# Kernel optimization log

Hardware: AMD Instinct MI355X
Metric: run time of the kernel (lower is better)

## Reference

```python
import jax, jax.numpy as jnp
import numpy as np

N_BLOCKS = 128
B0, B1 = 32, 32
COND_DIM = 0
IN_FEAT = B1 * N_BLOCKS + COND_DIM   # 4096
OUT_FEAT = B0 * N_BLOCKS             # 4096
BATCH = 2048


def _make_masks():
    # block-diagonal mask and strictly-lower block-triangular mask (int32)
    diag = np.kron(np.eye(N_BLOCKS, dtype=np.int32), np.ones((B0, B1), np.int32))
    tril = np.kron(np.tril(np.ones((N_BLOCKS, N_BLOCKS), np.int32), -1),
                   np.ones((B0, B1), np.int32))
    return jnp.asarray(diag), jnp.asarray(tril)


def setup_inputs() -> dict:
    key = jax.random.key(0)
    kx, kw, kb, ks = jax.random.split(key, 4)
    b_diag_mask, b_tril_mask = _make_masks()
    # glorot-like init, masked to the allowed sparsity pattern (as in __init__)
    scale = float(np.sqrt(2.0 / (IN_FEAT + OUT_FEAT)))
    W = jax.random.normal(kw, (OUT_FEAT, IN_FEAT), jnp.float32) * scale
    W = W * (b_diag_mask + b_tril_mask).astype(jnp.float32)
    bias = (jax.random.uniform(kb, (OUT_FEAT,), jnp.float32) - 0.5) * (2.0 / np.sqrt(OUT_FEAT))
    W_log_scale = jnp.log(jax.random.uniform(ks, (OUT_FEAT, 1), jnp.float32, 1e-3, 1.0))
    x = jax.random.normal(kx, (BATCH, IN_FEAT), jnp.float32)
    return {"x": x, "W": W, "bias": bias, "W_log_scale": W_log_scale,
            "b_diag_mask": b_diag_mask, "b_tril_mask": b_tril_mask}


def reference(x, W, bias, W_log_scale, b_diag_mask, b_tril_mask):
    dm = b_diag_mask.astype(W.dtype)
    tm = b_tril_mask.astype(W.dtype)
    # weight normalisation: exp on diag blocks, identity on tril blocks
    Wm = jnp.exp(W) * dm + W * tm
    W_norms = jnp.linalg.norm(Wm, axis=-1, keepdims=True)
    Wn = jnp.exp(W_log_scale) * Wm / W_norms           # (out, in)
    # batched y = Wn @ x + bias (per-sample vector matmul, batched)
    y = jnp.einsum("oi,bi->bo", Wn, x) + bias          # (batch, out)
    # gather diagonal blocks (row-major == jnp.where order in original)
    idx = jnp.arange(N_BLOCKS)
    Wb = Wn[:, COND_DIM:].reshape(N_BLOCKS, B0, N_BLOCKS, B1)
    jac_3d = Wb[idx, :, idx, :]                        # (n_blocks, B0, B1)
    return (y, jnp.log(jac_3d))
```

## Files before the change

### kernel.cpp

```cpp
#include <hip/hip_runtime.h>
#include <hip/hip_bf16.h>

typedef unsigned short u16;
using short8 = __attribute__((ext_vector_type(8))) short;
using f32x4  = __attribute__((ext_vector_type(4))) float;

#define IN_FEAT  4096
#define OUT_FEAT 4096
#define BATCH    2048
#define BPACK    8650752

#define GLOAD16(gp, lp)                                                        \
    __builtin_amdgcn_global_load_lds(                                          \
        (__attribute__((address_space(1))) void*)(gp),                         \
        (__attribute__((address_space(3))) void*)(lp), 16, 0, 0)

__global__ __launch_bounds__(256) void split_x(const float* __restrict__ x,
                                               u16* __restrict__ xhi,
                                               u16* __restrict__ xlo)
{
    const int n8 = (BATCH * IN_FEAT) / 8;
    for (int i = blockIdx.x * blockDim.x + threadIdx.x; i < n8;
         i += gridDim.x * blockDim.x) {
        float4 a = ((const float4*)x)[2 * i];
        float4 b = ((const float4*)x)[2 * i + 1];
        float vv[8] = {a.x, a.y, a.z, a.w, b.x, b.y, b.z, b.w};
        short8 h, l;
#pragma unroll
        for (int k = 0; k < 8; ++k) {
            __hip_bfloat16 hb = __float2bfloat16(vv[k]);
            float hf = __bfloat162float(hb);
            __hip_bfloat16 lb = __float2bfloat16(vv[k] - hf);
            h[k] = *(short*)&hb;
            l[k] = *(short*)&lb;
        }
        ((short8*)xhi)[i] = h;
        ((short8*)xlo)[i] = l;
    }
}

__global__ __launch_bounds__(256) void prep_w(const float* __restrict__ W,
                                              const float* __restrict__ wls,
                                              u16* __restrict__ bhi,
                                              u16* __restrict__ blo,
                                              float* __restrict__ jac)
{
    const int o    = 4095 - blockIdx.x;
    const int r    = o >> 5;
    const int g    = o >> 7;
    const int kact = (r + 1) * 32;
    const int kpad = (g + 1) << 7;
    const int dlo  = r * 32;

    __shared__ float rowbuf[4096];
    __shared__ float red[4];

    const float* wrow = W + (size_t)o * IN_FEAT;
    float ss = 0.f;
    const int k4 = kact >> 2;
    for (int c4 = threadIdx.x; c4 < k4; c4 += 256) {
        float4 wv = ((const float4*)wrow)[c4];
        f32x4 out;
        float vv[4] = {wv.x, wv.y, wv.z, wv.w};
        const int c = c4 * 4;
#pragma unroll
        for (int e = 0; e < 4; ++e) {
            float wm = (c + e >= dlo) ? __expf(vv[e]) : vv[e];
            out[e] = wm;
            ss += wm * wm;
        }
        *(f32x4*)&rowbuf[c] = out;
    }
    for (int off = 32; off > 0; off >>= 1) ss += __shfl_down(ss, off, 64);
    const int lane = threadIdx.x & 63, wid = threadIdx.x >> 6;
    if (lane == 0) red[wid] = ss;
    __syncthreads();
    const float total = red[0] + red[1] + red[2] + red[3];
    const float scale = expf(wls[o]) / sqrtf(total);

    const size_t rowbase = (size_t)16384 * ((size_t)g * (g + 1) / 2)
                         + (size_t)(o & 127) * kpad;
    u16* bh = bhi + rowbase;
    u16* bl = blo + rowbase;
    for (int c0 = threadIdx.x * 8; c0 < kpad; c0 += 2048) {
        short8 hv, lv;
        if (c0 + 8 <= kact) {
            f32x4 w0 = *(const f32x4*)&rowbuf[c0];
            f32x4 w1 = *(const f32x4*)&rowbuf[c0 + 4];
            float vv[8] = {w0[0], w0[1], w0[2], w0[3],
                           w1[0], w1[1], w1[2], w1[3]};
#pragma unroll
            for (int e = 0; e < 8; ++e) {
                float wn = vv[e] * scale;
                __hip_bfloat16 h = __float2bfloat16(wn);
                float hf = __bfloat162float(h);
                __hip_bfloat16 l = __float2bfloat16(wn - hf);
                hv[e] = *(short*)&h;
                lv[e] = *(short*)&l;
            }
        } else {
#pragma unroll
            for (int e = 0; e < 8; ++e) {
                const int c = c0 + e;
                float wn = (c < kact) ? rowbuf[c] * scale : 0.f;
                __hip_bfloat16 h = __float2bfloat16(wn);
                float hf = __bfloat162float(h);
                __hip_bfloat16 l = __float2bfloat16(wn - hf);
                hv[e] = *(short*)&h;
                lv[e] = *(short*)&l;
            }
        }
        *(short8*)(bh + c0) = hv;
        *(short8*)(bl + c0) = lv;
    }

    if (threadIdx.x < 32)
        jac[(size_t)r * 1024 + (size_t)(o & 31) * 32 + threadIdx.x] =
            __logf(rowbuf[dlo + threadIdx.x] * scale);
}

__global__ __launch_bounds__(256, 2) void gemm_bar(
    const u16* __restrict__ xhi, const u16* __restrict__ xlo,
    const u16* __restrict__ bhi, const u16* __restrict__ blo,
    const float* __restrict__ bias, float* __restrict__ y)
{
    __shared__ __align__(16) u16 As_hi[2][128][32];
    __shared__ __align__(16) u16 As_lo[2][128][32];
    __shared__ __align__(16) u16 Bs_hi[2][128][32];
    __shared__ __align__(16) u16 Bs_lo[2][128][32];

    const int bid = blockIdx.x;
    const int jj  = bid >> 4;
    const int j   = (jj < 16) ? (31 - jj) : (jj - 16);
    const int i   = bid & 15;
    const int bm0 = i * 128;
    const int bn0 = j * 128;
    const int ksteps = (j + 1) * 4;

    const int tid  = threadIdx.x;
    const int w    = tid >> 6;
    const int lane = tid & 63;
    const int wm   = (w & 1) * 64;
    const int wn   = (w >> 1) * 64;
    const int fr   = lane & 15;
    const int kq   = lane >> 4;
    const int kcg  = (kq ^ ((fr >> 1) & 3)) * 8;
    const int srr  = lane >> 2;
    const int scb  = ((lane & 3) ^ ((lane >> 3) & 3)) * 8;

    const u16* gbase;
    size_t gstride;
    u16* ldst0;
    if (w == 0) {
        gbase = xhi + (size_t)bm0 * IN_FEAT; gstride = IN_FEAT;
        ldst0 = &As_hi[0][0][0];
    } else if (w == 1) {
        gbase = xlo + (size_t)bm0 * IN_FEAT; gstride = IN_FEAT;
        ldst0 = &As_lo[0][0][0];
    } else {
        const size_t pbase = (size_t)16384 * ((size_t)j * (j + 1) / 2);
        gstride = (size_t)ksteps * 32;
        if (w == 2) { gbase = bhi + pbase; ldst0 = &Bs_hi[0][0][0]; }
        else        { gbase = blo + pbase; ldst0 = &Bs_lo[0][0][0]; }
    }

    f32x4 acc[4][4];
#pragma unroll
    for (int a = 0; a < 4; ++a)
#pragma unroll
        for (int b = 0; b < 4; ++b)
            acc[a][b] = (f32x4){0.f, 0.f, 0.f, 0.f};

#define STAGE(buf, kt)                                                         \
    do {                                                                       \
        const int _kb = (kt) * 32;                                             \
        u16* _dst = ldst0 + (buf) * 4096;                                      \
        _Pragma("unroll")                                                      \
        for (int _t = 0; _t < 8; ++_t) {                                       \
            const u16* _g = gbase + (size_t)(_t * 16 + srr) * gstride          \
                                  + _kb + scb;                                 \
            GLOAD16(_g, _dst + _t * 512);                                      \
        }                                                                      \
    } while (0)

    STAGE(0, 0);
    __syncthreads();

    int cur = 0;
    for (int kt = 0; kt < ksteps; ++kt) {
        if (kt + 1 < ksteps) STAGE(cur ^ 1, kt + 1);

        const int cb = cur * 4096;
        short8 ah[4], al[4], bh[4], bl[4];
#pragma unroll
        for (int mi = 0; mi < 4; ++mi) {
            const int row = wm + mi * 16 + fr;
            ah[mi] = *(const short8*)(&As_hi[0][0][0] + cb + row * 32 + kcg);
            al[mi] = *(const short8*)(&As_lo[0][0][0] + cb + row * 32 + kcg);
        }
#pragma unroll
        for (int ni = 0; ni < 4; ++ni) {
            const int row = wn + ni * 16 + fr;
            bh[ni] = *(const short8*)(&Bs_hi[0][0][0] + cb + row * 32 + kcg);
            bl[ni] = *(const short8*)(&Bs_lo[0][0][0] + cb + row * 32 + kcg);
        }
#pragma unroll
        for (int mi = 0; mi < 4; ++mi)
#pragma unroll
            for (int ni = 0; ni < 4; ++ni) {
                f32x4 c = acc[mi][ni];
                c = __builtin_amdgcn_mfma_f32_16x16x32_bf16(ah[mi], bh[ni], c, 0, 0, 0);
                c = __builtin_amdgcn_mfma_f32_16x16x32_bf16(ah[mi], bl[ni], c, 0, 0, 0);
                c = __builtin_amdgcn_mfma_f32_16x16x32_bf16(al[mi], bh[ni], c, 0, 0, 0);
                acc[mi][ni] = c;
            }
        __syncthreads();
        cur ^= 1;
    }
#undef STAGE

    const int crow = (lane >> 4) * 4;
    const int ccol = lane & 15;
#pragma unroll
    for (int ni = 0; ni < 4; ++ni) {
        const int n = bn0 + wn + ni * 16 + ccol;
        const float bv = bias[n];
#pragma unroll
        for (int mi = 0; mi < 4; ++mi) {
#pragma unroll
            for (int q = 0; q < 4; ++q) {
                const int m = bm0 + wm + mi * 16 + crow + q;
                y[(size_t)m * 4096 + n] = acc[mi][ni][q] + bv;
            }
        }
    }
}

extern "C" void kernel_launch(void* const* d_in, const int* in_sizes, int n_in,
                              void* d_out, int out_size, void* d_ws, size_t ws_size,
                              hipStream_t stream)
{
    const float* x    = (const float*)d_in[0];
    const float* W    = (const float*)d_in[1];
    const float* bias = (const float*)d_in[2];
    const float* wls  = (const float*)d_in[3];

    const size_t need = ((size_t)BPACK * 2 + (size_t)BATCH * IN_FEAT * 2)
                        * sizeof(u16);
    if (ws_size < need) return;

    u16* Bhi = (u16*)d_ws;
    u16* Blo = Bhi + (size_t)BPACK;
    u16* Xhi = Blo + (size_t)BPACK;
    u16* Xlo = Xhi + (size_t)BATCH * IN_FEAT;

    float* y   = (float*)d_out;
    float* jac = y + (size_t)BATCH * OUT_FEAT;

    split_x<<<1024, 256, 0, stream>>>(x, Xhi, Xlo);
    prep_w<<<4096, 256, 0, stream>>>(W, wls, Bhi, Blo, jac);
    gemm_bar<<<512, 256, 0, stream>>>(Xhi, Xlo, Bhi, Blo, bias, y);
}
```

Measured before the change: 310.3 us.

## Load A fragments directly from global into registers, stage only B in LDS

```diff
diff --git a/kernel.cpp b/kernel.cpp
--- a/kernel.cpp
+++ b/kernel.cpp
@@ -124,8 +124,6 @@
     const u16* __restrict__ bhi, const u16* __restrict__ blo,
     const float* __restrict__ bias, float* __restrict__ y)
 {
-    __shared__ __align__(16) u16 As_hi[2][128][32];
-    __shared__ __align__(16) u16 As_lo[2][128][32];
     __shared__ __align__(16) u16 Bs_hi[2][128][32];
     __shared__ __align__(16) u16 Bs_lo[2][128][32];
 
@@ -148,76 +146,90 @@
     const int srr  = lane >> 2;
     const int scb  = ((lane & 3) ^ ((lane >> 3) & 3)) * 8;
 
-    const u16* gbase;
-    size_t gstride;
-    u16* ldst0;
-    if (w == 0) {
-        gbase = xhi + (size_t)bm0 * IN_FEAT; gstride = IN_FEAT;
-        ldst0 = &As_hi[0][0][0];
-    } else if (w == 1) {
-        gbase = xlo + (size_t)bm0 * IN_FEAT; gstride = IN_FEAT;
-        ldst0 = &As_lo[0][0][0];
-    } else {
-        const size_t pbase = (size_t)16384 * ((size_t)j * (j + 1) / 2);
-        gstride = (size_t)ksteps * 32;
-        if (w == 2) { gbase = bhi + pbase; ldst0 = &Bs_hi[0][0][0]; }
-        else        { gbase = blo + pbase; ldst0 = &Bs_lo[0][0][0]; }
-    }
-
-    f32x4 acc[4][4];
-#pragma unroll
-    for (int a = 0; a < 4; ++a)
-#pragma unroll
-        for (int b = 0; b < 4; ++b)
-            acc[a][b] = (f32x4){0.f, 0.f, 0.f, 0.f};
-
-#define STAGE(buf, kt)                                                         \
+    const size_t pbase   = (size_t)16384 * ((size_t)j * (j + 1) / 2);
+    const size_t gstride = (size_t)ksteps * 32;
+    const u16* gsrcB = ((w >> 1) ? blo : bhi) + pbase;
+    u16* ldstB = (w >> 1) ? &Bs_lo[0][0][0] : &Bs_hi[0][0][0];
+    const int tbase = (w & 1) * 4;
+
+#define STAGE_B(buf, kt)                                                       \
     do {                                                                       \
         const int _kb = (kt) * 32;                                             \
-        u16* _dst = ldst0 + (buf) * 4096;                                      \
-        _Pragma("unroll")                                                      \
-        for (int _t = 0; _t < 8; ++_t) {                                       \
-            const u16* _g = gbase + (size_t)(_t * 16 + srr) * gstride          \
+        u16* _dst = ldstB + (buf) * 4096;                                      \
+        _Pragma("unroll")                                                      \
+        for (int _u = 0; _u < 4; ++_u) {                                       \
+            const int _t = tbase + _u;                                         \
+            const u16* _g = gsrcB + (size_t)(_t * 16 + srr) * gstride          \
                                   + _kb + scb;                                 \
             GLOAD16(_g, _dst + _t * 512);                                      \
         }                                                                      \
     } while (0)
 
-    STAGE(0, 0);
+    const u16* pAh = xhi + (size_t)(bm0 + wm + fr) * IN_FEAT + kq * 8;
+    const u16* pAl = xlo + (size_t)(bm0 + wm + fr) * IN_FEAT + kq * 8;
+
+#define LOAD_A(dh, dl, kt)                                                     \
+    do {                                                                       \
+        const size_t _o = (size_t)(kt) * 32;                                   \
+        _Pragma("unroll")                                                      \
+        for (int _mi = 0; _mi < 4; ++_mi) {                                    \
+            dh[_mi] = *(const short8*)(pAh + _o + (size_t)_mi * (16 * IN_FEAT));\
+            dl[_mi] = *(const short8*)(pAl + _o + (size_t)_mi * (16 * IN_FEAT));\
+        }                                                                      \
+    } while (0)
+
+#define COMPUTE(buf, ah, al)                                                   \
+    do {                                                                       \
+        const int _cb = (buf) * 4096;                                          \
+        short8 bhf[4], blf[4];                                                 \
+        _Pragma("unroll")                                                      \
+        for (int _ni = 0; _ni < 4; ++_ni) {                                    \
+            const int _row = wn + _ni * 16 + fr;                               \
+            bhf[_ni] = *(const short8*)(&Bs_hi[0][0][0] + _cb + _row * 32 + kcg);\
+            blf[_ni] = *(const short8*)(&Bs_lo[0][0][0] + _cb + _row * 32 + kcg);\
+        }                                                                      \
+        _Pragma("unroll")                                                      \
+        for (int _mi = 0; _mi < 4; ++_mi)                                      \
+            _Pragma("unroll")                                                  \
+            for (int _ni = 0; _ni < 4; ++_ni) {                                \
+                f32x4 _c = acc[_mi][_ni];                                      \
+                _c = __builtin_amdgcn_mfma_f32_16x16x32_bf16(ah[_mi], bhf[_ni], _c, 0, 0, 0);\
+                _c = __builtin_amdgcn_mfma_f32_16x16x32_bf16(ah[_mi], blf[_ni], _c, 0, 0, 0);\
+                _c = __builtin_amdgcn_mfma_f32_16x16x32_bf16(al[_mi], bhf[_ni], _c, 0, 0, 0);\
+                acc[_mi][_ni] = _c;                                            \
+            }                                                                  \
+    } while (0)
+
+    f32x4 acc[4][4];
+#pragma unroll
+    for (int a = 0; a < 4; ++a)
+#pragma unroll
+        for (int b = 0; b < 4; ++b)
+            acc[a][b] = (f32x4){0.f, 0.f, 0.f, 0.f};
+
+    short8 a0h[4], a0l[4], a1h[4], a1l[4];
+
+    STAGE_B(0, 0);
+    LOAD_A(a0h, a0l, 0);
     __syncthreads();
 
-    int cur = 0;
-    for (int kt = 0; kt < ksteps; ++kt) {
-        if (kt + 1 < ksteps) STAGE(cur ^ 1, kt + 1);
-
-        const int cb = cur * 4096;
-        short8 ah[4], al[4], bh[4], bl[4];
-#pragma unroll
-        for (int mi = 0; mi < 4; ++mi) {
-            const int row = wm + mi * 16 + fr;
-            ah[mi] = *(const short8*)(&As_hi[0][0][0] + cb + row * 32 + kcg);
-            al[mi] = *(const short8*)(&As_lo[0][0][0] + cb + row * 32 + kcg);
-        }
-#pragma unroll
-        for (int ni = 0; ni < 4; ++ni) {
-            const int row = wn + ni * 16 + fr;
-            bh[ni] = *(const short8*)(&Bs_hi[0][0][0] + cb + row * 32 + kcg);
-            bl[ni] = *(const short8*)(&Bs_lo[0][0][0] + cb + row * 32 + kcg);
-        }
-#pragma unroll
-        for (int mi = 0; mi < 4; ++mi)
-#pragma unroll
-            for (int ni = 0; ni < 4; ++ni) {
-                f32x4 c = acc[mi][ni];
-                c = __builtin_amdgcn_mfma_f32_16x16x32_bf16(ah[mi], bh[ni], c, 0, 0, 0);
-                c = __builtin_amdgcn_mfma_f32_16x16x32_bf16(ah[mi], bl[ni], c, 0, 0, 0);
-                c = __builtin_amdgcn_mfma_f32_16x16x32_bf16(al[mi], bh[ni], c, 0, 0, 0);
-                acc[mi][ni] = c;
-            }
+    for (int kt = 0; kt < ksteps; kt += 2) {
+        STAGE_B(1, kt + 1);
+        LOAD_A(a1h, a1l, kt + 1);
+        COMPUTE(0, a0h, a0l);
         __syncthreads();
-        cur ^= 1;
-    }
-#undef STAGE
+
+        const bool more = (kt + 2 < ksteps);
+        if (more) {
+            STAGE_B(0, kt + 2);
+            LOAD_A(a0h, a0l, kt + 2);
+        }
+        COMPUTE(1, a1h, a1l);
+        if (more) __syncthreads();
+    }
+#undef STAGE_B
+#undef LOAD_A
+#undef COMPUTE
 
     const int crow = (lane >> 4) * 4;
     const int ccol = lane & 15;
```

Measured after the change: 403.2 us. 30.0% more time.
